# Optimization experiments

Measured on AMD Instinct MI355X. Metric: run time of the kernel, lower is better.

The kernel has to match this reference:

```python
import jax, jax.numpy as jnp
import numpy as np

B, N, FEAT, HID, H = 4, 2048, 512, 512, 8
HD = HID // H  # head_dim = 64


def rotate_half(x):
    # pairs along last dim: (x1, x2) -> (-x2, x1), interleaved
    x = x.reshape(*x.shape[:-1], -1, 2)
    x1, x2 = x[..., 0], x[..., 1]
    return jnp.stack((-x2, x1), axis=-1).reshape(*x.shape[:-2], -1)


def apply_rope(freqs, t):
    # freqs: [2, B, 1, N, HD] broadcasting over heads; t: [B, H, N, HD]
    return t * freqs[0] + rotate_half(t) * freqs[1]


def setup_inputs() -> dict:
    key = jax.random.key(0)
    ks = jax.random.split(key, 12)
    s = 0.02
    return {
        "x0": jax.random.normal(ks[0], (B, N, FEAT), jnp.float32),
        "x1": jax.random.normal(ks[1], (B, N, FEAT), jnp.float32),
        "encoding0": jax.random.normal(ks[2], (2, B, 1, N, HD), jnp.float32),
        "encoding1": jax.random.normal(ks[3], (2, B, 1, N, HD), jnp.float32),
        "Wqkv": jax.random.normal(ks[4], (FEAT, 3 * HID), jnp.float32) * s,
        "bqkv": jnp.zeros((3 * HID,), jnp.float32),
        "Wproj": jax.random.normal(ks[5], (HID, HID), jnp.float32) * s,
        "bproj": jnp.zeros((HID,), jnp.float32),
        "W1": jax.random.normal(ks[6], (FEAT + HID, 2 * FEAT), jnp.float32) * s,
        "b1": jnp.zeros((2 * FEAT,), jnp.float32),
        "ln_g": jnp.ones((2 * FEAT,), jnp.float32),
        "ln_b": jnp.zeros((2 * FEAT,), jnp.float32),
        "W2": jax.random.normal(ks[7], (2 * FEAT, FEAT), jnp.float32) * s,
        "b2": jnp.zeros((FEAT,), jnp.float32),
    }


def _block(x, enc, Wqkv, bqkv, Wproj, bproj, W1, b1, ln_g, ln_b, W2, b2):
    b, n, _ = x.shape
    qkv = x @ Wqkv + bqkv                                   # [B,N,3*HID]
    qkv = qkv.reshape(b, n, H, HD, 3).transpose(0, 2, 1, 3, 4)  # [B,H,N,HD,3]
    q, k, v = qkv[..., 0], qkv[..., 1], qkv[..., 2]
    q = apply_rope(enc, q)
    k = apply_rope(enc, k)
    scale = q.shape[-1] ** (-0.5)
    attn = jax.nn.softmax(jnp.einsum('bhid,bhjd->bhij', q, k) * scale, axis=-1)
    o = jnp.einsum('bhij,bhjd->bhid', attn, v)              # [B,H,N,HD]
    message = o.transpose(0, 2, 1, 3).reshape(b, n, HID) @ Wproj + bproj
    h = jnp.concatenate([x, message], axis=-1) @ W1 + b1    # [B,N,2*FEAT]
    mu = h.mean(-1, keepdims=True)
    var = ((h - mu) ** 2).mean(-1, keepdims=True)
    h = (h - mu) * jax.lax.rsqrt(var + 1e-5) * ln_g + ln_b
    return x + jax.nn.gelu(h, approximate=False) @ W2 + b2


def reference(x0, x1, encoding0, encoding1, Wqkv, bqkv, Wproj, bproj, W1, b1, ln_g, ln_b, W2, b2):
    p = (Wqkv, bqkv, Wproj, bproj, W1, b1, ln_g, ln_b, W2, b2)
    return (_block(x0, encoding0, *p), _block(x1, encoding1, *p))
```

## Files before the change

### kernel.cpp

```cpp
#include <hip/hip_runtime.h>
#include <hip/hip_bf16.h>

typedef __attribute__((ext_vector_type(8))) short   short8v;
typedef __attribute__((ext_vector_type(4))) short   short4v;
typedef __attribute__((ext_vector_type(8))) __bf16  bf16x8;
typedef __attribute__((ext_vector_type(4))) __bf16  bf16x4;
typedef __attribute__((ext_vector_type(4))) float   f32x4;

constexpr int Nn = 2048;

#define GLOAD_LDS(src, dst) \
  __builtin_amdgcn_global_load_lds((__attribute__((address_space(1))) unsigned int*)(src), \
                                   (__attribute__((address_space(3))) unsigned int*)(dst), 16, 0, 0)

#if __has_builtin(__builtin_amdgcn_exp2f)
#define EXP2F(x) __builtin_amdgcn_exp2f(x)
#else
#define EXP2F(x) exp2f(x)
#endif

#if __has_builtin(__builtin_amdgcn_mfma_f32_16x16x16bf16_1k)
#define HAVE_MFMA16 1
#define MFMA16(a, b, c) __builtin_amdgcn_mfma_f32_16x16x16bf16_1k(a, b, c, 0, 0, 0)
#else
#define HAVE_MFMA16 0
#endif

__device__ __forceinline__ unsigned pack_bf16(float lo, float hi) {
  union { __bf16 h[2]; unsigned u; } t;
  t.h[0] = (__bf16)lo; t.h[1] = (__bf16)hi;
  return t.u;
}

template<int AMODE, int EPI>
__global__ __launch_bounds__(256)
void gemm_mfma(const __bf16* __restrict__ A, const __bf16* __restrict__ A2,
               const __bf16* __restrict__ BT,
               const float* __restrict__ bias,
               const float* __restrict__ resid0, const float* __restrict__ resid1,
               float* __restrict__ Cf, __bf16* __restrict__ Cb, __bf16* __restrict__ Vt,
               int lda, int ldb, int ldc, int K1, int K)
{
  __shared__ __align__(16) __bf16 As[128 * 32];
  __shared__ __align__(16) __bf16 Bs[128 * 32];
  const int tid = threadIdx.x;
  const int w = tid >> 6, l = tid & 63;
  const int wr = w >> 1, wc = w & 1;
  const int lr = l & 15, lg = l >> 4;
  const int row0 = blockIdx.x * 128, col0 = blockIdx.y * 128;

  f32x4 acc[4][4];
#pragma unroll
  for (int i = 0; i < 4; ++i)
#pragma unroll
    for (int j = 0; j < 4; ++j) acc[i][j] = (f32x4){0.f, 0.f, 0.f, 0.f};

  const int srow = l >> 2;
  const int skk  = (l & 3) * 8;

  for (int k0 = 0; k0 < K; k0 += 32) {
    for (int s = w; s < 8; s += 4) {
      const int m = s * 16 + srow;
      const __bf16* src;
      if constexpr (AMODE == 0) {
        src = A + (size_t)(row0 + m) * lda + k0 + skk;
      } else {
        const int gk = k0 + skk;
        src = (gk < K1) ? A  + (size_t)(row0 + m) * lda + gk
                        : A2 + (size_t)(row0 + m) * lda + (gk - K1);
      }
      GLOAD_LDS(src, &As[s * 512]);
    }
    for (int s = w; s < 8; s += 4) {
      const int n = s * 16 + srow;
      GLOAD_LDS(BT + (size_t)(col0 + n) * ldb + k0 + skk, &Bs[s * 512]);
    }
    __syncthreads();
    bf16x8 af[4], bfv[4];
#pragma unroll
    for (int mi = 0; mi < 4; ++mi)
      af[mi] = *(const bf16x8*)&As[(wr * 64 + mi * 16 + lr) * 32 + lg * 8];
#pragma unroll
    for (int ni = 0; ni < 4; ++ni)
      bfv[ni] = *(const bf16x8*)&Bs[(wc * 64 + ni * 16 + lr) * 32 + lg * 8];
    __builtin_amdgcn_s_setprio(1);
#pragma unroll
    for (int mi = 0; mi < 4; ++mi)
#pragma unroll
      for (int ni = 0; ni < 4; ++ni)
        acc[mi][ni] = __builtin_amdgcn_mfma_f32_16x16x32_bf16(af[mi], bfv[ni], acc[mi][ni], 0, 0, 0);
    __builtin_amdgcn_s_setprio(0);
    __syncthreads();
  }

  if constexpr (EPI == 4) {
    if (col0 >= 1024) {
      const int b2 = row0 >> 11;
#pragma unroll
      for (int mi = 0; mi < 4; ++mi)
#pragma unroll
        for (int ni = 0; ni < 4; ++ni) {
          const int col = col0 + wc * 64 + ni * 16 + lr;
          const int sec = col - 1024, h = sec >> 6, d = sec & 63;
          const int n0 = (row0 + wr * 64 + mi * 16 + lg * 4) & 2047;
          union { __bf16 h4[4]; short4 s4; } u;
#pragma unroll
          for (int r = 0; r < 4; ++r) u.h4[r] = (__bf16)(acc[mi][ni][r] + bias[col]);
          *(short4*)&Vt[(size_t)(b2 * 8 + h) * 131072 + (size_t)d * 2048 + n0] = u.s4;
        }
    } else {
#pragma unroll
      for (int mi = 0; mi < 4; ++mi)
#pragma unroll
        for (int ni = 0; ni < 4; ++ni) {
          const int col = col0 + wc * 64 + ni * 16 + lr;
#pragma unroll
          for (int r = 0; r < 4; ++r) {
            const int row = row0 + wr * 64 + mi * 16 + lg * 4 + r;
            Cb[(size_t)row * 1024 + col] = (__bf16)(acc[mi][ni][r] + bias[col]);
          }
        }
    }
    return;
  }

#pragma unroll
  for (int mi = 0; mi < 4; ++mi)
#pragma unroll
    for (int ni = 0; ni < 4; ++ni) {
      const int col = col0 + wc * 64 + ni * 16 + lr;
#pragma unroll
      for (int r = 0; r < 4; ++r) {
        const int row = row0 + wr * 64 + mi * 16 + lg * 4 + r;
        const float v = acc[mi][ni][r];
        if constexpr (EPI == 1) {
          Cb[(size_t)row * ldc + col] = (__bf16)(v + bias[col]);
        } else {
          const float* rp = (row < 8192) ? resid0 : resid1;
          Cf[(size_t)row * ldc + col] = v + bias[col] + rp[(size_t)(row & 8191) * ldc + col];
        }
      }
    }
}

__global__ __launch_bounds__(256, 2)
void fa_k(const __bf16* __restrict__ QK, const __bf16* __restrict__ Vg,
          __bf16* __restrict__ Ob)
{
  __shared__ __align__(16) __bf16 Ks[2][8192];
  __shared__ __align__(16) __bf16 Vs[2][8192];
  const int tid = threadIdx.x;
  const int w = tid >> 6, l = tid & 63;
  const int lr = l & 15, lg = l >> 4;
  const int bh = blockIdx.y;
  const int b2 = bh >> 3, h = bh & 7;
  const __bf16* Qp = QK + (size_t)b2 * 2048 * 1024 + h * 64;
  const __bf16* Kp = Qp + 512;
  const __bf16* Vp = Vg + (size_t)bh * 131072;
  const int q0 = blockIdx.x * 128 + w * 32;

  bf16x8 qf[2][2];
#pragma unroll
  for (int nf = 0; nf < 2; ++nf)
#pragma unroll
    for (int kk = 0; kk < 2; ++kk)
      qf[nf][kk] = *(const bf16x8*)&Qp[(size_t)(q0 + nf * 16 + lr) * 1024 + kk * 32 + lg * 8];

  f32x4 oacc[4][2];
#pragma unroll
  for (int i = 0; i < 4; ++i)
#pragma unroll
    for (int j = 0; j < 2; ++j) oacc[i][j] = (f32x4){0.f, 0.f, 0.f, 0.f};
  float m_run[2] = {-1e30f, -1e30f}, lsum[2] = {0.f, 0.f};

#if !HAVE_MFMA16
  const int Sa = (lg & 1) * 32 + lr, Sb2x = Sa + 16;
  const bool hi = (lg >> 1) & 1;
#endif

  auto stage = [&](int kv0, int b) {
#pragma unroll
    for (int i = 0; i < 4; ++i) {
      const int s = w + 4 * i;
      { const int g = s * 64 + l, r = g >> 3, c = g & 7;
        GLOAD_LDS(Kp + (size_t)(kv0 + r) * 1024 + ((c ^ (r & 7)) * 8), &Ks[b][s * 512]); }
      { const int g = s * 64 + l, r = g >> 4, c = g & 15;
        GLOAD_LDS(Vp + (size_t)r * 2048 + kv0 + ((c ^ (r & 15)) * 8), &Vs[b][s * 512]); }
    }
  };

  stage(0, 0);

  for (int t = 0; t < 16; ++t) {
    const int p = t & 1;
    if (t < 15) {
      stage((t + 1) * 128, 1 - p);
      asm volatile("s_waitcnt vmcnt(8)" ::: "memory");
    } else {
      asm volatile("s_waitcnt vmcnt(0)" ::: "memory");
    }
    __builtin_amdgcn_sched_barrier(0);
    __builtin_amdgcn_s_barrier();
    __builtin_amdgcn_sched_barrier(0);

    f32x4 sacc[8][2];
#pragma unroll
    for (int i = 0; i < 8; ++i)
#pragma unroll
      for (int j = 0; j < 2; ++j) sacc[i][j] = (f32x4){0.f, 0.f, 0.f, 0.f};
#pragma unroll
    for (int kk = 0; kk < 2; ++kk) {
      bf16x8 ka[8];
#pragma unroll
      for (int mf = 0; mf < 8; ++mf)
        ka[mf] = *(const bf16x8*)&Ks[p][(mf * 16 + lr) * 64 + (((kk * 4 + lg) ^ (lr & 7)) * 8)];
      __builtin_amdgcn_s_setprio(1);
#pragma unroll
      for (int mf = 0; mf < 8; ++mf)
#pragma unroll
        for (int nf = 0; nf < 2; ++nf)
          sacc[mf][nf] = __builtin_amdgcn_mfma_f32_16x16x32_bf16(ka[mf], qf[nf][kk], sacc[mf][nf], 0, 0, 0);
      __builtin_amdgcn_s_setprio(0);
    }

    unsigned pkk[8][2][2];
#pragma unroll
    for (int nf = 0; nf < 2; ++nf) {
      float tm = -1e30f;
#pragma unroll
      for (int mf = 0; mf < 8; ++mf)
#pragma unroll
        for (int r = 0; r < 4; ++r) tm = fmaxf(tm, sacc[mf][nf][r]);
      tm = fmaxf(tm, __shfl_xor(tm, 16, 64));
      tm = fmaxf(tm, __shfl_xor(tm, 32, 64));
      if (__any(tm > m_run[nf] + 8.f)) {
        const float mn = fmaxf(m_run[nf], tm);
        const float corr = EXP2F(m_run[nf] - mn);
        m_run[nf] = mn;
        lsum[nf] *= corr;
#pragma unroll
        for (int mo = 0; mo < 4; ++mo)
#pragma unroll
          for (int r = 0; r < 4; ++r) oacc[mo][nf][r] *= corr;
      }
      const float mcur = m_run[nf];
      float rs = 0.f;
#pragma unroll
      for (int mf = 0; mf < 8; ++mf) {
        const float p0 = EXP2F(sacc[mf][nf][0] - mcur);
        const float p1 = EXP2F(sacc[mf][nf][1] - mcur);
        const float p2 = EXP2F(sacc[mf][nf][2] - mcur);
        const float p3 = EXP2F(sacc[mf][nf][3] - mcur);
        rs += (p0 + p1) + (p2 + p3);
        pkk[mf][nf][0] = pack_bf16(p0, p1);
        pkk[mf][nf][1] = pack_bf16(p2, p3);
      }
      rs += __shfl_xor(rs, 16, 64);
      rs += __shfl_xor(rs, 32, 64);
      lsum[nf] += rs;
    }

#if HAVE_MFMA16
#pragma unroll
    for (int ks = 0; ks < 8; ++ks) {
      bf16x4 va[4];
#pragma unroll
      for (int mo = 0; mo < 4; ++mo) {
        const int og = 2 * ks + (lg >> 1);
        va[mo] = *(const bf16x4*)&Vs[p][(mo * 16 + lr) * 128 + ((og ^ lr) & 15) * 8 + (lg & 1) * 4];
      }
      __builtin_amdgcn_s_setprio(1);
#pragma unroll
      for (int mo = 0; mo < 4; ++mo)
#pragma unroll
        for (int nf = 0; nf < 2; ++nf)
          oacc[mo][nf] = MFMA16(__builtin_bit_cast(short4v, va[mo]),
                                __builtin_bit_cast(short4v, pkk[ks][nf]),
                                oacc[mo][nf]);
      __builtin_amdgcn_s_setprio(0);
    }
#else
#pragma unroll
    for (int kf = 0; kf < 4; ++kf) {
      bf16x8 va[4];
#pragma unroll
      for (int mo = 0; mo < 4; ++mo)
        va[mo] = *(const bf16x8*)&Vs[p][(mo * 16 + lr) * 128 + ((((kf * 4 + lg) ^ lr) & 15) * 8)];
      bf16x8 bfr[2];
#pragma unroll
      for (int nf = 0; nf < 2; ++nf) {
        const unsigned s0 = hi ? pkk[kf * 2 + 1][nf][0] : pkk[kf * 2][nf][0];
        const unsigned s1 = hi ? pkk[kf * 2 + 1][nf][1] : pkk[kf * 2][nf][1];
        union { unsigned u[4]; bf16x8 v; } ub;
        ub.u[0] = (unsigned)__shfl((int)s0, Sa, 64);
        ub.u[1] = (unsigned)__shfl((int)s1, Sa, 64);
        ub.u[2] = (unsigned)__shfl((int)s0, Sb2x, 64);
        ub.u[3] = (unsigned)__shfl((int)s1, Sb2x, 64);
        bfr[nf] = ub.v;
      }
      __builtin_amdgcn_s_setprio(1);
#pragma unroll
      for (int mo = 0; mo < 4; ++mo)
#pragma unroll
        for (int nf = 0; nf < 2; ++nf)
          oacc[mo][nf] = __builtin_amdgcn_mfma_f32_16x16x32_bf16(va[mo], bfr[nf], oacc[mo][nf], 0, 0, 0);
      __builtin_amdgcn_s_setprio(0);
    }
#endif
    __builtin_amdgcn_s_barrier();
  }

#pragma unroll
  for (int nf = 0; nf < 2; ++nf) {
    const float inv = 1.f / lsum[nf];
    const long row = (long)b2 * 2048 + q0 + nf * 16 + lr;
#pragma unroll
    for (int mo = 0; mo < 4; ++mo) {
      union { __bf16 h4[4]; short4 s4; } u;
#pragma unroll
      for (int r = 0; r < 4; ++r) u.h4[r] = (__bf16)(oacc[mo][nf][r] * inv);
      *(short4*)&Ob[row * 512 + h * 64 + mo * 16 + lg * 4] = u.s4;
    }
  }
}

__global__ __launch_bounds__(256)
void conv_f32_bf16_k(const float* __restrict__ s, __bf16* __restrict__ d)
{
  const long i = ((long)blockIdx.x * 256 + threadIdx.x) * 4;
  const float4 v = *(const float4*)&s[i];
  union { __bf16 h[4]; short4 sv; } u;
  u.h[0] = (__bf16)v.x; u.h[1] = (__bf16)v.y; u.h[2] = (__bf16)v.z; u.h[3] = (__bf16)v.w;
  *(short4*)&d[i] = u.sv;
}

template<int PERM>
__global__ __launch_bounds__(256)
void transpose_wt_k(const float* __restrict__ W, __bf16* __restrict__ WT, int K, int N)
{
  __shared__ float t[32][33];
  const int n0 = blockIdx.x * 32, k0 = blockIdx.y * 32;
  const int tx = threadIdx.x & 31, ty = threadIdx.x >> 5;
  for (int i = ty; i < 32; i += 8)
    t[i][tx] = W[(size_t)(k0 + i) * N + n0 + tx];
  __syncthreads();
  for (int i = ty; i < 32; i += 8) {
    int drow = n0 + i;
    if constexpr (PERM) {
      const int h = drow / 192, rem = drow % 192;
      drow = (rem % 3) * 512 + h * 64 + rem / 3;
    }
    WT[(size_t)drow * K + k0 + tx] = (__bf16)t[tx][i];
  }
}

__global__ void bperm_k(const float* __restrict__ b, float* __restrict__ bp)
{
  const int i = blockIdx.x * 256 + threadIdx.x;
  if (i < 1536) {
    const int h = i / 192, rem = i % 192;
    bp[(rem % 3) * 512 + h * 64 + rem / 3] = b[i];
  }
}

__global__ __launch_bounds__(256)
void rope_k(__bf16* __restrict__ qkvb, const float* __restrict__ enc0,
            const float* __restrict__ enc1)
{
  constexpr float SCQ = 0.125f * 1.44269504089f;
  const long idx = (long)blockIdx.x * 256 + threadIdx.x;
  const int t = (int)(idx & 31);
  const int h = (int)((idx >> 5) & 7);
  const long row = idx >> 8;
  const long bn = row & 8191;
  const float* e = (row < 8192) ? enc0 : enc1;
  const int d0 = 2 * t;
  const float f0a = e[bn * 64 + d0], f0b = e[bn * 64 + d0 + 1];
  const float f1a = e[524288 + bn * 64 + d0], f1b = e[524288 + bn * 64 + d0 + 1];
  const long base = row * 1024 + (long)h * 64 + d0;
  {
    union { __bf16 hx[2]; unsigned u; } p;
    p.u = *(unsigned*)&qkvb[base];
    const float x0 = (float)p.hx[0], x1 = (float)p.hx[1];
    p.hx[0] = (__bf16)((x0 * f0a - x1 * f1a) * SCQ);
    p.hx[1] = (__bf16)((x1 * f0b + x0 * f1b) * SCQ);
    *(unsigned*)&qkvb[base] = p.u;
  }
  {
    union { __bf16 hx[2]; unsigned u; } p;
    p.u = *(unsigned*)&qkvb[base + 512];
    const float x0 = (float)p.hx[0], x1 = (float)p.hx[1];
    p.hx[0] = (__bf16)(x0 * f0a - x1 * f1a);
    p.hx[1] = (__bf16)(x1 * f0b + x0 * f1b);
    *(unsigned*)&qkvb[base + 512] = p.u;
  }
}

__global__ __launch_bounds__(256)
void ln_gelu_k(__bf16* __restrict__ Hb, const float* __restrict__ g,
               const float* __restrict__ be)
{
  __bf16* row = Hb + (size_t)blockIdx.x * 1024;
  const int tid = threadIdx.x;
  __shared__ float rs_[256], rq_[256];
  union { __bf16 h[4]; short4 sv; } u;
  u.sv = *(const short4*)&row[tid * 4];
  float v[4];
  float s = 0.f, sq = 0.f;
#pragma unroll
  for (int i = 0; i < 4; ++i) {
    v[i] = (float)u.h[i];
    s += v[i]; sq += v[i] * v[i];
  }
  rs_[tid] = s; rq_[tid] = sq; __syncthreads();
  for (int st = 128; st > 0; st >>= 1) {
    if (tid < st) { rs_[tid] += rs_[tid + st]; rq_[tid] += rq_[tid + st]; }
    __syncthreads();
  }
  const float mu = rs_[0] * (1.f / 1024.f);
  const float var = rq_[0] * (1.f / 1024.f) - mu * mu;
  const float rstd = rsqrtf(var + 1e-5f);
#pragma unroll
  for (int i = 0; i < 4; ++i) {
    const int c = tid * 4 + i;
    const float y = (v[i] - mu) * rstd * g[c] + be[c];
    u.h[i] = (__bf16)(0.5f * y * (1.f + erff(y * 0.70710678118f)));
  }
  *(short4*)&row[tid * 4] = u.sv;
}

extern "C" void kernel_launch(void* const* d_in, const int* in_sizes, int n_in,
                              void* d_out, int out_size, void* d_ws, size_t ws_size,
                              hipStream_t stream)
{
  const float* x0   = (const float*)d_in[0];
  const float* x1   = (const float*)d_in[1];
  const float* enc0 = (const float*)d_in[2];
  const float* enc1 = (const float*)d_in[3];
  const float* Wqkv  = (const float*)d_in[4];
  const float* bqkv  = (const float*)d_in[5];
  const float* Wproj = (const float*)d_in[6];
  const float* bproj = (const float*)d_in[7];
  const float* W1    = (const float*)d_in[8];
  const float* b1    = (const float*)d_in[9];
  const float* ln_g  = (const float*)d_in[10];
  const float* ln_b  = (const float*)d_in[11];
  const float* W2    = (const float*)d_in[12];
  const float* b2    = (const float*)d_in[13];

  __bf16* wsb = (__bf16*)d_ws;
  __bf16* xb     = wsb;
  __bf16* WqkvT  = wsb + 8388608;
  __bf16* WprojT = wsb + 9175040;
  __bf16* W1T    = wsb + 9437184;
  __bf16* W2T    = wsb + 10485760;
  float*  bqkvp  = (float*)(wsb + 11010048);
  __bf16* qkvb   = wsb + 11013120;
  __bf16* Vt     = wsb + 27790336;
  __bf16* Ob     = wsb + 36178944;
  __bf16* msgb   = qkvb;
  __bf16* hb     = Vt;

  transpose_wt_k<1><<<dim3(48, 16), 256, 0, stream>>>(Wqkv, WqkvT, 512, 1536);
  transpose_wt_k<0><<<dim3(16, 16), 256, 0, stream>>>(Wproj, WprojT, 512, 512);
  transpose_wt_k<0><<<dim3(32, 32), 256, 0, stream>>>(W1, W1T, 1024, 1024);
  transpose_wt_k<0><<<dim3(16, 32), 256, 0, stream>>>(W2, W2T, 1024, 512);
  bperm_k<<<6, 256, 0, stream>>>(bqkv, bqkvp);

  conv_f32_bf16_k<<<4096, 256, 0, stream>>>(x0, xb);
  conv_f32_bf16_k<<<4096, 256, 0, stream>>>(x1, xb + 4194304);

  gemm_mfma<0, 4><<<dim3(128, 12), 256, 0, stream>>>(
      xb, nullptr, WqkvT, bqkvp, nullptr, nullptr, nullptr, qkvb, Vt,
      512, 512, 1024, 0, 512);
  rope_k<<<16384, 256, 0, stream>>>(qkvb, enc0, enc1);
  fa_k<<<dim3(16, 64), 256, 0, stream>>>(qkvb, Vt, Ob);
  gemm_mfma<0, 1><<<dim3(128, 4), 256, 0, stream>>>(
      Ob, nullptr, WprojT, bproj, nullptr, nullptr, nullptr, msgb, nullptr,
      512, 512, 512, 0, 512);
  gemm_mfma<1, 1><<<dim3(128, 8), 256, 0, stream>>>(
      xb, msgb, W1T, b1, nullptr, nullptr, nullptr, hb, nullptr,
      512, 1024, 1024, 512, 1024);
  ln_gelu_k<<<16384, 256, 0, stream>>>(hb, ln_g, ln_b);
  gemm_mfma<0, 2><<<dim3(128, 4), 256, 0, stream>>>(
      hb, nullptr, W2T, b2, x0, x1, (float*)d_out, nullptr, nullptr,
      1024, 1024, 512, 0, 1024);
}
```

Baseline: 353.6 us.

## Fold Wproj into W1 and double-buffer GEMM LDS tiles

Precomputes a fused weight (the message half of W1 composed with Wproj) plus a fused bias, so the projection GEMM is removed and the W1 GEMM reads the attention output directly through a second B operand. The GEMM kernel also gains double-buffered LDS staging, with the next tile's loads issued before computing on the current one, using explicit vmcnt waits and raw barriers. The fused weight is stored in bf16 after an extra rounding, which may change numerics slightly. It also adds small per-call setup kernels for the weight fusion.

```diff
diff --git a/kernel.cpp b/kernel.cpp
--- a/kernel.cpp
+++ b/kernel.cpp
@@ -32,17 +32,17 @@
   return t.u;
 }
 
-template<int AMODE, int EPI>
+template<int AMODE, int BMODE, int EPI>
 __global__ __launch_bounds__(256)
 void gemm_mfma(const __bf16* __restrict__ A, const __bf16* __restrict__ A2,
-               const __bf16* __restrict__ BT,
+               const __bf16* __restrict__ BT, const __bf16* __restrict__ BT2,
                const float* __restrict__ bias,
                const float* __restrict__ resid0, const float* __restrict__ resid1,
                float* __restrict__ Cf, __bf16* __restrict__ Cb, __bf16* __restrict__ Vt,
-               int lda, int ldb, int ldc, int K1, int K)
-{
-  __shared__ __align__(16) __bf16 As[128 * 32];
-  __shared__ __align__(16) __bf16 Bs[128 * 32];
+               int lda, int ldb, int ldb2, int ldc, int K1, int K)
+{
+  __shared__ __align__(16) __bf16 As[2][4096];
+  __shared__ __align__(16) __bf16 Bs[2][4096];
   const int tid = threadIdx.x;
   const int w = tid >> 6, l = tid & 63;
   const int wr = w >> 1, wc = w & 1;
@@ -58,7 +58,8 @@
   const int srow = l >> 2;
   const int skk  = (l & 3) * 8;
 
-  for (int k0 = 0; k0 < K; k0 += 32) {
+  auto stage = [&](int k0, int b) {
+#pragma unroll
     for (int s = w; s < 8; s += 4) {
       const int m = s * 16 + srow;
       const __bf16* src;
@@ -69,20 +70,44 @@
         src = (gk < K1) ? A  + (size_t)(row0 + m) * lda + gk
                         : A2 + (size_t)(row0 + m) * lda + (gk - K1);
       }
-      GLOAD_LDS(src, &As[s * 512]);
-    }
+      GLOAD_LDS(src, &As[b][s * 512]);
+    }
+#pragma unroll
     for (int s = w; s < 8; s += 4) {
       const int n = s * 16 + srow;
-      GLOAD_LDS(BT + (size_t)(col0 + n) * ldb + k0 + skk, &Bs[s * 512]);
-    }
-    __syncthreads();
+      const __bf16* src;
+      if constexpr (BMODE == 0) {
+        src = BT + (size_t)(col0 + n) * ldb + k0 + skk;
+      } else {
+        const int gk = k0 + skk;
+        src = (gk < K1) ? BT  + (size_t)(col0 + n) * ldb + gk
+                        : BT2 + (size_t)(col0 + n) * ldb2 + (gk - K1);
+      }
+      GLOAD_LDS(src, &Bs[b][s * 512]);
+    }
+  };
+
+  const int nt = K >> 5;
+  stage(0, 0);
+
+  for (int t = 0; t < nt; ++t) {
+    const int p = t & 1;
+    if (t + 1 < nt) {
+      stage((t + 1) * 32, 1 - p);
+      asm volatile("s_waitcnt vmcnt(4)" ::: "memory");
+    } else {
+      asm volatile("s_waitcnt vmcnt(0)" ::: "memory");
+    }
+    __builtin_amdgcn_sched_barrier(0);
+    __builtin_amdgcn_s_barrier();
+    __builtin_amdgcn_sched_barrier(0);
     bf16x8 af[4], bfv[4];
 #pragma unroll
     for (int mi = 0; mi < 4; ++mi)
-      af[mi] = *(const bf16x8*)&As[(wr * 64 + mi * 16 + lr) * 32 + lg * 8];
+      af[mi] = *(const bf16x8*)&As[p][(wr * 64 + mi * 16 + lr) * 32 + lg * 8];
 #pragma unroll
     for (int ni = 0; ni < 4; ++ni)
-      bfv[ni] = *(const bf16x8*)&Bs[(wc * 64 + ni * 16 + lr) * 32 + lg * 8];
+      bfv[ni] = *(const bf16x8*)&Bs[p][(wc * 64 + ni * 16 + lr) * 32 + lg * 8];
     __builtin_amdgcn_s_setprio(1);
 #pragma unroll
     for (int mi = 0; mi < 4; ++mi)
@@ -90,7 +115,7 @@
       for (int ni = 0; ni < 4; ++ni)
         acc[mi][ni] = __builtin_amdgcn_mfma_f32_16x16x32_bf16(af[mi], bfv[ni], acc[mi][ni], 0, 0, 0);
     __builtin_amdgcn_s_setprio(0);
-    __syncthreads();
+    __builtin_amdgcn_s_barrier();
   }
 
   if constexpr (EPI == 4) {
@@ -135,6 +160,8 @@
         const float v = acc[mi][ni][r];
         if constexpr (EPI == 1) {
           Cb[(size_t)row * ldc + col] = (__bf16)(v + bias[col]);
+        } else if constexpr (EPI == 3) {
+          Cb[(size_t)row * ldc + col] = (__bf16)v;
         } else {
           const float* rp = (row < 8192) ? resid0 : resid1;
           Cf[(size_t)row * ldc + col] = v + bias[col] + rp[(size_t)(row & 8191) * ldc + col];
@@ -361,6 +388,17 @@
     const int h = i / 192, rem = i % 192;
     bp[(rem % 3) * 512 + h * 64 + rem / 3] = b[i];
   }
+}
+
+__global__ __launch_bounds__(256)
+void bfuse_k(const float* __restrict__ b1, const float* __restrict__ bproj,
+             const float* __restrict__ W1, float* __restrict__ b1f)
+{
+  const int n = blockIdx.x * 256 + threadIdx.x;
+  float s = b1[n];
+  for (int m = 0; m < 512; ++m)
+    s += bproj[m] * W1[(size_t)(512 + m) * 1024 + n];
+  b1f[n] = s;
 }
 
 __global__ __launch_bounds__(256)
@@ -449,40 +487,42 @@
   const float* b2    = (const float*)d_in[13];
 
   __bf16* wsb = (__bf16*)d_ws;
-  __bf16* xb     = wsb;
-  __bf16* WqkvT  = wsb + 8388608;
-  __bf16* WprojT = wsb + 9175040;
-  __bf16* W1T    = wsb + 9437184;
-  __bf16* W2T    = wsb + 10485760;
-  float*  bqkvp  = (float*)(wsb + 11010048);
-  __bf16* qkvb   = wsb + 11013120;
-  __bf16* Vt     = wsb + 27790336;
-  __bf16* Ob     = wsb + 36178944;
-  __bf16* msgb   = qkvb;
-  __bf16* hb     = Vt;
+  __bf16* xb      = wsb;
+  __bf16* WqkvT   = wsb + 8388608;
+  __bf16* Wproj_b = wsb + 9175040;
+  __bf16* W1T     = wsb + 9437184;
+  __bf16* W2T     = wsb + 10485760;
+  float*  bqkvp   = (float*)(wsb + 11010048);
+  __bf16* qkvb    = wsb + 11013120;
+  __bf16* Vt      = wsb + 27790336;
+  __bf16* Ob      = wsb + 36178944;
+  __bf16* WfT     = wsb + 44567552;
+  float*  b1f     = (float*)(wsb + 45091840);
+  __bf16* hb      = qkvb;
 
   transpose_wt_k<1><<<dim3(48, 16), 256, 0, stream>>>(Wqkv, WqkvT, 512, 1536);
-  transpose_wt_k<0><<<dim3(16, 16), 256, 0, stream>>>(Wproj, WprojT, 512, 512);
   transpose_wt_k<0><<<dim3(32, 32), 256, 0, stream>>>(W1, W1T, 1024, 1024);
   transpose_wt_k<0><<<dim3(16, 32), 256, 0, stream>>>(W2, W2T, 1024, 512);
   bperm_k<<<6, 256, 0, stream>>>(bqkv, bqkvp);
+  conv_f32_bf16_k<<<256, 256, 0, stream>>>(Wproj, Wproj_b);
+  gemm_mfma<0, 0, 3><<<dim3(8, 4), 256, 0, stream>>>(
+      W1T + 512, nullptr, Wproj_b, nullptr, nullptr, nullptr, nullptr,
+      nullptr, WfT, nullptr, 1024, 512, 0, 512, 0, 512);
+  bfuse_k<<<4, 256, 0, stream>>>(b1, bproj, W1, b1f);
 
   conv_f32_bf16_k<<<4096, 256, 0, stream>>>(x0, xb);
   conv_f32_bf16_k<<<4096, 256, 0, stream>>>(x1, xb + 4194304);
 
-  gemm_mfma<0, 4><<<dim3(128, 12), 256, 0, stream>>>(
-      xb, nullptr, WqkvT, bqkvp, nullptr, nullptr, nullptr, qkvb, Vt,
-      512, 512, 1024, 0, 512);
+  gemm_mfma<0, 0, 4><<<dim3(128, 12), 256, 0, stream>>>(
+      xb, nullptr, WqkvT, nullptr, bqkvp, nullptr, nullptr, nullptr, qkvb, Vt,
+      512, 512, 0, 1024, 0, 512);
   rope_k<<<16384, 256, 0, stream>>>(qkvb, enc0, enc1);
   fa_k<<<dim3(16, 64), 256, 0, stream>>>(qkvb, Vt, Ob);
-  gemm_mfma<0, 1><<<dim3(128, 4), 256, 0, stream>>>(
-      Ob, nullptr, WprojT, bproj, nullptr, nullptr, nullptr, msgb, nullptr,
-      512, 512, 512, 0, 512);
-  gemm_mfma<1, 1><<<dim3(128, 8), 256, 0, stream>>>(
-      xb, msgb, W1T, b1, nullptr, nullptr, nullptr, hb, nullptr,
-      512, 1024, 1024, 512, 1024);
+  gemm_mfma<1, 1, 1><<<dim3(128, 8), 256, 0, stream>>>(
+      xb, Ob, W1T, WfT, b1f, nullptr, nullptr, nullptr, hb, nullptr,
+      512, 1024, 512, 1024, 512, 1024);
   ln_gelu_k<<<16384, 256, 0, stream>>>(hb, ln_g, ln_b);
-  gemm_mfma<0, 2><<<dim3(128, 4), 256, 0, stream>>>(
-      hb, nullptr, W2T, b2, x0, x1, (float*)d_out, nullptr, nullptr,
-      1024, 1024, 512, 0, 1024);
-}
+  gemm_mfma<0, 0, 2><<<dim3(128, 4), 256, 0, stream>>>(
+      hb, nullptr, W2T, nullptr, b2, x0, x1, (float*)d_out, nullptr, nullptr,
+      1024, 1024, 0, 512, 0, 1024);
+}
```

Result: faster. 346.0 us (-2.1%).
